# Optimization experiments

Hardware: AMD Instinct MI355X
Metric: run time of the kernel (lower is better)

Reference implementation:

```python
import jax, jax.numpy as jnp
import numpy as np

B, E, N, D = 32, 16384, 1000, 128


def setup_inputs() -> dict:
    key = jax.random.key(0)
    ks = jax.random.split(key, 8)
    s = 1.0 / np.sqrt(D)
    return {
        "edge_attr": jax.random.normal(ks[0], (B, E, D), dtype=jnp.float32),
        "edge_index": jax.random.randint(ks[1], (B, 2, E), 0, N, dtype=jnp.int32),
        "W1": jax.random.uniform(ks[2], (D, D), jnp.float32, -s, s),
        "b1": jax.random.uniform(ks[3], (D,), jnp.float32, -s, s),
        "W2": jax.random.uniform(ks[4], (D, D), jnp.float32, -s, s),
        "b2": jax.random.uniform(ks[5], (D,), jnp.float32, -s, s),
        "Wo": jax.random.uniform(ks[6], (1, D), jnp.float32, -s, s),
        "bo": jax.random.uniform(ks[7], (1,), jnp.float32, -s, s),
    }


def reference(edge_attr, edge_index, W1, b1, W2, b2, Wo, bo):
    # MLP over edge features: two hidden silu layers then sigmoid output * 10
    h = jax.nn.silu(jnp.einsum("bed,kd->bek", edge_attr, W1) + b1)
    h = jax.nn.silu(jnp.einsum("bed,kd->bek", h, W2) + b2)
    vals = jax.nn.sigmoid(jnp.einsum("bed,kd->bek", h, Wo) + bo)[..., 0] * 10.0  # [B, E]

    src = edge_index[:, 0, :]  # [B, E]
    dst = edge_index[:, 1, :]  # [B, E]
    b_idx = jnp.arange(B, dtype=edge_index.dtype)[:, None]  # [B, 1]
    heat = jnp.zeros((B, N, N), dtype=edge_attr.dtype).at[b_idx, src, dst].set(vals)

    # undirected_graph=True: symmetrize
    return (heat + jnp.swapaxes(heat, 1, 2)) * 0.5
```

## Files before the change

### kernel.cpp

```cpp
#include <hip/hip_runtime.h>
#include <hip/hip_bf16.h>
#include <math.h>

#define B_ 32
#define E_ 16384
#define N_ 1000
#define D_ 128
#define NN_ (N_ * N_)
#define T_ 8

typedef __attribute__((ext_vector_type(8))) short bf16x8;
typedef __attribute__((ext_vector_type(4))) float f32x4;

__device__ __forceinline__ unsigned short f2bf(float f) {
    unsigned u = __float_as_uint(f);
    u += 0x7FFFu + ((u >> 16) & 1u);
    return (unsigned short)(u >> 16);
}

__device__ __forceinline__ unsigned pk2(float lo, float hi) {
    __hip_bfloat162 h = __float22bfloat162_rn(make_float2(lo, hi));
    return *(unsigned*)&h;
}

__device__ __forceinline__ f32x4 mfma16(bf16x8 a, bf16x8 b, f32x4 c) {
    return __builtin_amdgcn_mfma_f32_16x16x32_bf16(a, b, c, 0, 0, 0);
}

__device__ __forceinline__ float silu_(float z) {
    return z * __builtin_amdgcn_rcpf(1.0f + __expf(-z));
}

__device__ __forceinline__ float dec17(unsigned x) {
    return (float)((x & 0x1FFFFu) - 1u) * (10.0f / 131070.0f);
}

__device__ __forceinline__ void gload_lds16(const void* g, void* l) {
    __builtin_amdgcn_global_load_lds(
        (const __attribute__((address_space(1))) unsigned*)g,
        (__attribute__((address_space(3))) unsigned*)l, 16, 0, 0);
}

__global__ __launch_bounds__(256) void fill_and_prep(
    uint4* __restrict__ p, int n4,
    const float* __restrict__ W1, const float* __restrict__ W2,
    unsigned short* __restrict__ wsz)
{
    if (blockIdx.x < 128) {
        int t = blockIdx.x * 256 + threadIdx.x;
        int w = t >> 14, e = t & 16383;
        int row = e >> 7, pos = e & 127;
        int src_col = pos;
        if (w) {
            int q = pos >> 5, gg = (pos >> 3) & 3, nn = (pos >> 2) & 1, r = pos & 3;
            src_col = (q * 2 + nn) * 16 + gg * 4 + r;
        }
        float v = (w ? W2 : W1)[row * 128 + src_col];
        char* dst = (char*)wsz + (size_t)w * 32768 + row * 256 +
                    ((pos * 2) ^ ((row & 7) << 4));
        *(unsigned short*)dst = f2bf(v);
    }
    int i = blockIdx.x * 256 + threadIdx.x;
    const int stride = gridDim.x * 256;
    const uint4 z = make_uint4(0u, 0u, 0u, 0u);
    for (; i < n4; i += stride) p[i] = z;
}

__global__ __launch_bounds__(256, 2) void mlp_scatter_kernel(
    const float* __restrict__ X, const int* __restrict__ EI,
    const unsigned short* __restrict__ wsz,
    const float* __restrict__ b1, const float* __restrict__ b2,
    const float* __restrict__ Wo, const float* __restrict__ bo,
    unsigned* __restrict__ out)
{
    __shared__ __align__(16) char Wb[65536];
    __shared__ __align__(16) float BiasL[388];

    const int tid = threadIdx.x;
    const int lane = tid & 63;
    const int wv = tid >> 6;
    const int l15 = lane & 15;
    const int g = (lane >> 4) & 3;

    const int bb = blockIdx.x >> 4;
    const int e0 = (blockIdx.x & 15) * (128 * T_);

    if (tid < 96) {
        const float* src = tid < 32 ? b1 : (tid < 64 ? b2 : Wo);
        ((f32x4*)BiasL)[tid] = ((const f32x4*)src)[tid & 31];
    }
    if (tid == 96) BiasL[384] = bo[0];

    float4 af[2][4][2];
    auto load_af = [&](int stv) {
        #pragma unroll
        for (int m = 0; m < 2; ++m) {
            const float* p0 = X + ((size_t)bb * E_ + e0 + stv * 128 + wv * 32 +
                                   m * 16 + l15) * D_ + g * 8;
            #pragma unroll
            for (int ks = 0; ks < 4; ++ks) {
                af[m][ks][0] = *(const float4*)(p0 + ks * 32);
                af[m][ks][1] = *(const float4*)(p0 + ks * 32 + 4);
            }
        }
    };

    load_af(0);

    #pragma unroll
    for (int it = 0; it < 16; ++it) {
        int off = it * 4096 + tid * 16;
        gload_lds16((const char*)wsz + off, (char*)Wb + off);
    }
    __syncthreads();
    const float bo0 = BiasL[384];

    #pragma unroll 1
    for (int st = 0; st < T_; ++st) {
        const int eb0 = e0 + st * 128 + wv * 32;

        int eisv[2], eidv[2];
        #pragma unroll
        for (int m = 0; m < 2; ++m) {
            int e = eb0 + m * 16 + l15;
            eisv[m] = EI[(size_t)bb * 2 * E_ + e];
            eidv[m] = EI[(size_t)bb * 2 * E_ + E_ + e];
        }

        bf16x8 a[2][4];
        #pragma unroll
        for (int m = 0; m < 2; ++m)
            #pragma unroll
            for (int ks = 0; ks < 4; ++ks) {
                bf16x8 t; unsigned* tu = (unsigned*)&t;
                tu[0] = pk2(af[m][ks][0].x, af[m][ks][0].y);
                tu[1] = pk2(af[m][ks][0].z, af[m][ks][0].w);
                tu[2] = pk2(af[m][ks][1].x, af[m][ks][1].y);
                tu[3] = pk2(af[m][ks][1].z, af[m][ks][1].w);
                a[m][ks] = t;
            }

        if (st + 1 < T_) load_af(st + 1);

        bf16x8 pa[2][4];
        #pragma unroll
        for (int q = 0; q < 4; ++q) {
            f32x4 acc1[2][2];
            #pragma unroll
            for (int m = 0; m < 2; ++m) {
                acc1[m][0] = (f32x4){0.f, 0.f, 0.f, 0.f};
                acc1[m][1] = (f32x4){0.f, 0.f, 0.f, 0.f};
            }
            #pragma unroll
            for (int ks = 0; ks < 4; ++ks)
                #pragma unroll
                for (int nn = 0; nn < 2; ++nn) {
                    int row = l15 + (q * 2 + nn) * 16;
                    bf16x8 aw = *(const bf16x8*)(Wb + row * 256 +
                                  ((ks * 64 + g * 16) ^ ((row & 7) << 4)));
                    acc1[0][nn] = mfma16(aw, a[0][ks], acc1[0][nn]);
                    acc1[1][nn] = mfma16(aw, a[1][ks], acc1[1][nn]);
                }
            f32x4 b1q0 = ((f32x4*)BiasL)[(q * 2 + 0) * 4 + g];
            f32x4 b1q1 = ((f32x4*)BiasL)[(q * 2 + 1) * 4 + g];
            #pragma unroll
            for (int m = 0; m < 2; ++m) {
                unsigned* au = (unsigned*)&pa[m][q];
                au[0] = pk2(silu_(acc1[m][0][0] + b1q0[0]), silu_(acc1[m][0][1] + b1q0[1]));
                au[1] = pk2(silu_(acc1[m][0][2] + b1q0[2]), silu_(acc1[m][0][3] + b1q0[3]));
                au[2] = pk2(silu_(acc1[m][1][0] + b1q1[0]), silu_(acc1[m][1][1] + b1q1[1]));
                au[3] = pk2(silu_(acc1[m][1][2] + b1q1[2]), silu_(acc1[m][1][3] + b1q1[3]));
            }
            __builtin_amdgcn_sched_barrier(0);
        }

        float zed[2] = {0.f, 0.f};
        #pragma unroll
        for (int nh = 0; nh < 2; ++nh) {
            f32x4 acc2[2][4];
            #pragma unroll
            for (int m = 0; m < 2; ++m)
                #pragma unroll
                for (int n = 0; n < 4; ++n)
                    acc2[m][n] = (f32x4){0.f, 0.f, 0.f, 0.f};

            #pragma unroll
            for (int q = 0; q < 4; ++q) {
                #pragma unroll
                for (int n = 0; n < 4; ++n) {
                    int row = l15 + (nh * 4 + n) * 16;
                    bf16x8 w2 = *(const bf16x8*)(Wb + 32768 + row * 256 +
                                  ((q * 64 + g * 16) ^ ((row & 7) << 4)));
                    acc2[0][n] = mfma16(w2, pa[0][q], acc2[0][n]);
                    acc2[1][n] = mfma16(w2, pa[1][q], acc2[1][n]);
                }
                __builtin_amdgcn_sched_barrier(0);
            }

            #pragma unroll
            for (int n = 0; n < 4; ++n) {
                int nn = nh * 4 + n;
                f32x4 b2q = ((f32x4*)BiasL)[32 + nn * 4 + g];
                f32x4 woq = ((f32x4*)BiasL)[64 + nn * 4 + g];
                #pragma unroll
                for (int m = 0; m < 2; ++m) {
                    zed[m] += silu_(acc2[m][n][0] + b2q[0]) * woq[0];
                    zed[m] += silu_(acc2[m][n][1] + b2q[1]) * woq[1];
                    zed[m] += silu_(acc2[m][n][2] + b2q[2]) * woq[2];
                    zed[m] += silu_(acc2[m][n][3] + b2q[3]) * woq[3];
                }
            }
        }

        #pragma unroll
        for (int m = 0; m < 2; ++m) {
            zed[m] += __shfl_xor(zed[m], 16, 64);
            zed[m] += __shfl_xor(zed[m], 32, 64);
        }

        if (g == 0) {
            #pragma unroll
            for (int m = 0; m < 2; ++m) {
                int e = eb0 + m * 16 + l15;
                float z = zed[m] + bo0;
                float val = 10.0f * __builtin_amdgcn_rcpf(1.0f + __expf(-z));
                unsigned qv = (unsigned)(val * 13107.0f + 0.5f) + 1u;
                if (qv > 0x1FFFFu) qv = 0x1FFFFu;
                unsigned packed = 0x80000000u | ((unsigned)e << 17) | qv;
                atomicMax(out + ((size_t)bb * NN_ + (size_t)eisv[m] * N_ + eidv[m]),
                          packed);
            }
        }
    }
}

__global__ __launch_bounds__(256) void finalize_fused(
    const int* __restrict__ EI, unsigned* __restrict__ out)
{
    int i = blockIdx.x * 256 + threadIdx.x;
    int b = i >> 14, e = i & 16383;
    int s = EI[(size_t)b * 2 * E_ + e];
    int d = EI[(size_t)b * 2 * E_ + E_ + e];
    unsigned* ob = out + (size_t)b * NN_;
    unsigned x1 = ob[(size_t)s * N_ + d];
    unsigned x2 = ob[(size_t)d * N_ + s];
    float v;
    if (!(x1 >> 31) && x1)      v = __uint_as_float(x1);
    else if (!(x2 >> 31) && x2) v = __uint_as_float(x2);
    else {
        float c1 = (x1 >> 31) ? dec17(x1) : 0.0f;
        float c2 = (x2 >> 31) ? dec17(x2) : 0.0f;
        v = 0.5f * (c1 + c2);
    }
    unsigned uv = __float_as_uint(v);
    ob[(size_t)s * N_ + d] = uv;
    ob[(size_t)d * N_ + s] = uv;
}

extern "C" void kernel_launch(void* const* d_in, const int* in_sizes, int n_in,
                              void* d_out, int out_size, void* d_ws, size_t ws_size,
                              hipStream_t stream) {
    const float* X  = (const float*)d_in[0];
    const int*   EI = (const int*)d_in[1];
    const float* W1 = (const float*)d_in[2];
    const float* b1 = (const float*)d_in[3];
    const float* W2 = (const float*)d_in[4];
    const float* b2 = (const float*)d_in[5];
    const float* Wo = (const float*)d_in[6];
    const float* bo = (const float*)d_in[7];
    unsigned* out = (unsigned*)d_out;
    unsigned short* wsz = (unsigned short*)d_ws;

    fill_and_prep<<<dim3(2048), dim3(256), 0, stream>>>(
        (uint4*)d_out, out_size / 4, W1, W2, wsz);
    mlp_scatter_kernel<<<dim3((B_ * E_) / (128 * T_)), dim3(256), 0, stream>>>(
        X, EI, wsz, b1, b2, Wo, bo, out);
    finalize_fused<<<dim3((B_ * E_) / 256), dim3(256), 0, stream>>>(EI, out);
}
```

Baseline: 143.4 us.

## Deepen X prefetch pipeline, stage edge indices in LDS, retile second GEMM

Restructures the edge-tile loop into pairs with separate half-tile register buffers, so loads for future tiles are issued earlier and more global loads stay in flight behind the MFMA work. Edge indices for the block are bulk-copied into LDS once instead of being read from global memory in every iteration. The second GEMM is split into four smaller quarters with fewer accumulators, which lowers register pressure. The copies into the extra prefetch buffers raise register use and could spill or cut occupancy at two waves per SIMD.

Result: no change. 146.1 us (+1.8%).

```diff
diff --git a/kernel.cpp b/kernel.cpp
--- a/kernel.cpp
+++ b/kernel.cpp
@@ -74,6 +74,7 @@
     unsigned* __restrict__ out)
 {
     __shared__ __align__(16) char Wb[65536];
+    __shared__ __align__(16) int  EIl[2048];
     __shared__ __align__(16) float BiasL[388];
 
     const int tid = threadIdx.x;
@@ -91,56 +92,50 @@
     }
     if (tid == 96) BiasL[384] = bo[0];
 
-    float4 af[2][4][2];
-    auto load_af = [&](int stv) {
-        #pragma unroll
-        for (int m = 0; m < 2; ++m) {
-            const float* p0 = X + ((size_t)bb * E_ + e0 + stv * 128 + wv * 32 +
-                                   m * 16 + l15) * D_ + g * 8;
-            #pragma unroll
-            for (int ks = 0; ks < 4; ++ks) {
-                af[m][ks][0] = *(const float4*)(p0 + ks * 32);
-                af[m][ks][1] = *(const float4*)(p0 + ks * 32 + 4);
-            }
+    auto load_half = [&](float4 (&buf)[4][2], int stv, int mm) {
+        const float* p0 = X + ((size_t)bb * E_ + e0 + stv * 128 + wv * 32 +
+                               mm * 16 + l15) * D_ + g * 8;
+        #pragma unroll
+        for (int ks = 0; ks < 4; ++ks) {
+            buf[ks][0] = *(const float4*)(p0 + ks * 32);
+            buf[ks][1] = *(const float4*)(p0 + ks * 32 + 4);
         }
     };
 
-    load_af(0);
+    float4 P0[4][2], P1[4][2], Q[4][2];
+    load_half(P0, 0, 0);
+    load_half(P1, 1, 0);
+    load_half(Q, 0, 1);
 
     #pragma unroll
     for (int it = 0; it < 16; ++it) {
         int off = it * 4096 + tid * 16;
         gload_lds16((const char*)wsz + off, (char*)Wb + off);
     }
+    gload_lds16((const char*)(EI + (size_t)bb * 2 * E_ + e0) + tid * 16,
+                (char*)EIl + tid * 16);
+    gload_lds16((const char*)(EI + (size_t)bb * 2 * E_ + E_ + e0) + tid * 16,
+                (char*)EIl + 4096 + tid * 16);
     __syncthreads();
     const float bo0 = BiasL[384];
 
-    #pragma unroll 1
-    for (int st = 0; st < T_; ++st) {
-        const int eb0 = e0 + st * 128 + wv * 32;
-
-        int eisv[2], eidv[2];
-        #pragma unroll
-        for (int m = 0; m < 2; ++m) {
-            int e = eb0 + m * 16 + l15;
-            eisv[m] = EI[(size_t)bb * 2 * E_ + e];
-            eidv[m] = EI[(size_t)bb * 2 * E_ + E_ + e];
-        }
-
+    auto body = [&](float4 (&m0buf)[4][2], float4 (&m1buf)[4][2], int st) {
         bf16x8 a[2][4];
         #pragma unroll
-        for (int m = 0; m < 2; ++m)
-            #pragma unroll
-            for (int ks = 0; ks < 4; ++ks) {
-                bf16x8 t; unsigned* tu = (unsigned*)&t;
-                tu[0] = pk2(af[m][ks][0].x, af[m][ks][0].y);
-                tu[1] = pk2(af[m][ks][0].z, af[m][ks][0].w);
-                tu[2] = pk2(af[m][ks][1].x, af[m][ks][1].y);
-                tu[3] = pk2(af[m][ks][1].z, af[m][ks][1].w);
-                a[m][ks] = t;
-            }
-
-        if (st + 1 < T_) load_af(st + 1);
+        for (int ks = 0; ks < 4; ++ks) {
+            bf16x8 t0; unsigned* u0 = (unsigned*)&t0;
+            u0[0] = pk2(m0buf[ks][0].x, m0buf[ks][0].y);
+            u0[1] = pk2(m0buf[ks][0].z, m0buf[ks][0].w);
+            u0[2] = pk2(m0buf[ks][1].x, m0buf[ks][1].y);
+            u0[3] = pk2(m0buf[ks][1].z, m0buf[ks][1].w);
+            a[0][ks] = t0;
+            bf16x8 t1; unsigned* u1 = (unsigned*)&t1;
+            u1[0] = pk2(m1buf[ks][0].x, m1buf[ks][0].y);
+            u1[1] = pk2(m1buf[ks][0].z, m1buf[ks][0].w);
+            u1[2] = pk2(m1buf[ks][1].x, m1buf[ks][1].y);
+            u1[3] = pk2(m1buf[ks][1].z, m1buf[ks][1].w);
+            a[1][ks] = t1;
+        }
 
         bf16x8 pa[2][4];
         #pragma unroll
@@ -176,30 +171,28 @@
 
         float zed[2] = {0.f, 0.f};
         #pragma unroll
-        for (int nh = 0; nh < 2; ++nh) {
-            f32x4 acc2[2][4];
-            #pragma unroll
-            for (int m = 0; m < 2; ++m)
-                #pragma unroll
-                for (int n = 0; n < 4; ++n)
-                    acc2[m][n] = (f32x4){0.f, 0.f, 0.f, 0.f};
-
+        for (int nq = 0; nq < 4; ++nq) {
+            f32x4 acc2[2][2];
+            #pragma unroll
+            for (int m = 0; m < 2; ++m) {
+                acc2[m][0] = (f32x4){0.f, 0.f, 0.f, 0.f};
+                acc2[m][1] = (f32x4){0.f, 0.f, 0.f, 0.f};
+            }
             #pragma unroll
             for (int q = 0; q < 4; ++q) {
                 #pragma unroll
-                for (int n = 0; n < 4; ++n) {
-                    int row = l15 + (nh * 4 + n) * 16;
+                for (int n = 0; n < 2; ++n) {
+                    int row = l15 + (nq * 2 + n) * 16;
                     bf16x8 w2 = *(const bf16x8*)(Wb + 32768 + row * 256 +
                                   ((q * 64 + g * 16) ^ ((row & 7) << 4)));
                     acc2[0][n] = mfma16(w2, pa[0][q], acc2[0][n]);
                     acc2[1][n] = mfma16(w2, pa[1][q], acc2[1][n]);
                 }
-                __builtin_amdgcn_sched_barrier(0);
-            }
-
-            #pragma unroll
-            for (int n = 0; n < 4; ++n) {
-                int nn = nh * 4 + n;
+            }
+            __builtin_amdgcn_sched_barrier(0);
+            #pragma unroll
+            for (int n = 0; n < 2; ++n) {
+                int nn = nq * 2 + n;
                 f32x4 b2q = ((f32x4*)BiasL)[32 + nn * 4 + g];
                 f32x4 woq = ((f32x4*)BiasL)[64 + nn * 4 + g];
                 #pragma unroll
@@ -221,15 +214,47 @@
         if (g == 0) {
             #pragma unroll
             for (int m = 0; m < 2; ++m) {
-                int e = eb0 + m * 16 + l15;
+                int el = st * 128 + wv * 32 + m * 16 + l15;
+                int s = EIl[el];
+                int d = EIl[1024 + el];
                 float z = zed[m] + bo0;
                 float val = 10.0f * __builtin_amdgcn_rcpf(1.0f + __expf(-z));
                 unsigned qv = (unsigned)(val * 13107.0f + 0.5f) + 1u;
                 if (qv > 0x1FFFFu) qv = 0x1FFFFu;
-                unsigned packed = 0x80000000u | ((unsigned)e << 17) | qv;
-                atomicMax(out + ((size_t)bb * NN_ + (size_t)eisv[m] * N_ + eidv[m]),
-                          packed);
-            }
+                unsigned packed = 0x80000000u | ((unsigned)(e0 + el) << 17) | qv;
+                atomicMax(out + ((size_t)bb * NN_ + (size_t)s * N_ + d), packed);
+            }
+        }
+    };
+
+    #pragma unroll 1
+    for (int stp = 0; stp < T_ / 2; ++stp) {
+        const int st = 2 * stp;
+        {
+            bf16x8 dummy;
+            (void)dummy;
+        }
+        {
+            float4 sP0[4][2], sQ[4][2];
+            #pragma unroll
+            for (int ks = 0; ks < 4; ++ks) {
+                sP0[ks][0] = P0[ks][0]; sP0[ks][1] = P0[ks][1];
+                sQ[ks][0]  = Q[ks][0];  sQ[ks][1]  = Q[ks][1];
+            }
+            if (st + 2 < T_) load_half(P0, st + 2, 0);
+            load_half(Q, st + 1, 1);
+            body(sP0, sQ, st);
+        }
+        {
+            float4 sP1[4][2], sQ[4][2];
+            #pragma unroll
+            for (int ks = 0; ks < 4; ++ks) {
+                sP1[ks][0] = P1[ks][0]; sP1[ks][1] = P1[ks][1];
+                sQ[ks][0]  = Q[ks][0];  sQ[ks][1]  = Q[ks][1];
+            }
+            if (st + 3 < T_) load_half(P1, st + 3, 0);
+            if (st + 2 < T_) load_half(Q, st + 2, 1);
+            body(sP1, sQ, st + 1);
         }
     }
 }
```
